# Performance work log

Hardware: AMD Instinct MI355X
Metric: run time of the kernel (lower is better)

Reference implementation:

```python
import jax, jax.numpy as jnp
import numpy as np

B, T, IN = 128, 2048, 32      # batch, seq_len, input dim
S, M = 32, 8                  # kaarma state dim, number of ensemble models
E, H = 64, 128                # encoder dim, controller GRU hidden
CIN = E + 1                   # controller input = [encoded, error]


def setup_inputs() -> dict:
    key = jax.random.key(0)
    ks = jax.random.split(key, 15)
    sc = 0.1  # small init scale keeps tanh/sigmoid in sane range
    return {
        "x": jax.random.normal(ks[0], (B, T, IN), jnp.float32),
        "y": jax.random.normal(ks[1], (B, T), jnp.float32),
        # mkaarma params: shared encoder + per-model recurrent state update
        "W_enc": jax.random.normal(ks[2], (IN, E), jnp.float32) * sc,
        "b_enc": jnp.zeros((E,), jnp.float32),
        "W_in": jax.random.normal(ks[3], (M, IN, S), jnp.float32) * sc,
        "W_rec": jax.random.normal(ks[4], (M, S, S), jnp.float32) * sc,
        "b_s": jnp.zeros((M, S), jnp.float32),
        # controller params: GRU cell + gate head
        "W_x": jax.random.normal(ks[5], (CIN, 3 * H), jnp.float32) * sc,
        "W_h": jax.random.normal(ks[6], (H, 3 * H), jnp.float32) * sc,
        "b_x": jnp.zeros((3 * H,), jnp.float32),
        "b_h": jnp.zeros((3 * H,), jnp.float32),
        "W_gate": jax.random.normal(ks[7], (H, M), jnp.float32) * sc,
        "b_gate": jnp.zeros((M,), jnp.float32),
    }


def reference(x, y, W_enc, b_enc, W_in, W_rec, b_s,
              W_x, W_h, b_x, b_h, W_gate, b_gate):
    Bv = x.shape[0]
    dt = x.dtype

    def step(carry, xy):
        kstate, h, err = carry            # [B,S], [B,H], [B]
        x_t, y_t = xy                     # [B,IN], [B]
        # mkaarma: encode input + ensemble of candidate next states
        encoded = jnp.tanh(x_t @ W_enc + b_enc)                        # [B,E]
        new_state = jnp.tanh(
            jnp.einsum('bi,mis->bms', x_t, W_in)
            + jnp.einsum('bs,msd->bmd', kstate, W_rec)
            + b_s
        )                                                              # [B,M,S]
        # controller: GRU cell on [encoded, error]
        inp = jnp.concatenate([encoded, err[:, None]], axis=1)         # [B,E+1]
        xz, xr, xn = jnp.split(inp @ W_x + b_x, 3, axis=1)
        hz, hr, hn = jnp.split(h @ W_h + b_h, 3, axis=1)
        z = jax.nn.sigmoid(xz + hz)
        r = jax.nn.sigmoid(xr + hr)
        n = jnp.tanh(xn + r * hn)
        h_new = (1.0 - z) * n + z * h                                  # [B,H]
        # gate softmax over models, mix candidate states
        gate = jax.nn.softmax(h_new @ W_gate + b_gate, axis=1)         # [B,M]
        kstate_new = jnp.einsum('bm,bms->bs', gate, new_state)         # [B,S]
        pred = kstate_new[:, -1]                                       # [B]
        err_new = pred - y_t
        return (kstate_new, h_new, err_new), pred

    init = (jnp.zeros((Bv, S), dt), jnp.zeros((Bv, H), dt), jnp.zeros((Bv,), dt))
    xs = (jnp.swapaxes(x, 0, 1), jnp.swapaxes(y, 0, 1))   # time-major
    _, preds = jax.lax.scan(step, init, xs)               # [T,B]
    return jnp.swapaxes(preds, 0, 1)                      # [B,T]
```

## Files before the change

### kernel.cpp

```cpp
#include <hip/hip_runtime.h>

typedef _Float16 h2 __attribute__((ext_vector_type(2)));
typedef _Float16 h8 __attribute__((ext_vector_type(8)));

#define NB 128
#define NT 2048
#define NIN 32
#define NS 32
#define NM 8
#define NE 64
#define NH 128
#define NH3 384

__device__ __forceinline__ h2 mkh2(float a, float b) {
  h2 r; r[0] = (_Float16)a; r[1] = (_Float16)b; return r;
}

template <int I>
__device__ __forceinline__ h2 pick2(h8 v) {
  return __builtin_shufflevector(v, v, 2 * I, 2 * I + 1);
}

__device__ __forceinline__ float fdot2(h2 a, h2 b, float c) {
#if __has_builtin(__builtin_amdgcn_fdot2)
  return __builtin_amdgcn_fdot2(a, b, c, false);
#else
  return c + (float)a[0] * (float)b[0] + (float)a[1] * (float)b[1];
#endif
}

__device__ __forceinline__ float rcpf(float v) {
#if __has_builtin(__builtin_amdgcn_rcpf)
  return __builtin_amdgcn_rcpf(v);
#else
  return 1.0f / v;
#endif
}

__device__ __forceinline__ float sigmoid_f(float v) { return rcpf(1.0f + __expf(-v)); }
__device__ __forceinline__ float tanh_f(float v) { return 1.0f - 2.0f * rcpf(1.0f + __expf(2.0f * v)); }

template <int CTRL>
__device__ __forceinline__ float dppadd(float v) {
  int t = __builtin_amdgcn_update_dpp(0, __float_as_int(v), CTRL, 0xF, 0xF, true);
  return v + __int_as_float(t);
}
__device__ __forceinline__ float wave_reduce63(float v) {
  v = dppadd<0x111>(v); v = dppadd<0x112>(v); v = dppadd<0x114>(v);
  v = dppadd<0x118>(v); v = dppadd<0x142>(v); v = dppadd<0x143>(v);
  return v;
}
__device__ __forceinline__ float pairsum(float v) {
  int t = __builtin_amdgcn_update_dpp(0, __float_as_int(v), 0xB1, 0xF, 0xF, true);
  return v + __int_as_float(t);
}

__device__ __forceinline__ void lds_fence() {
  asm volatile("s_waitcnt lgkmcnt(0)" ::: "memory");
}

__device__ __forceinline__ void softbar() {
  asm volatile("s_waitcnt lgkmcnt(0)\n\ts_barrier" ::: "memory");
}

#define RPW 16
__global__ __launch_bounds__(256, 1) void pre2(
    const float* __restrict__ gx, const float* __restrict__ W_enc,
    const float* __restrict__ b_enc, const float* __restrict__ W_x,
    const float* __restrict__ b_x, _Float16* __restrict__ xpre,
    _Float16* __restrict__ xh16, int t0, int CH) {
  const int tid = threadIdx.x, wv = tid >> 6, lane = tid & 63;
  __shared__ __align__(16) _Float16 x16[4][NIN];
  __shared__ __align__(16) _Float16 encA[4][RPW][NE];

  h2 we[16];
#pragma unroll
  for (int i = 0; i < 16; ++i)
    we[i] = mkh2(W_enc[(2 * i) * NE + lane], W_enc[(2 * i + 1) * NE + lane]);
  const float be = b_enc[lane];

  const int g0 = ((int)blockIdx.x * 4 + wv) * RPW;

  h2 wx3[96];
#pragma unroll 1
  for (int pass = 0; pass < 2; ++pass) {
#pragma unroll
    for (int kk = 0; kk < 3; ++kk) {
      const int j = lane + 64 * (3 * pass + kk);
#pragma unroll
      for (int i = 0; i < 32; ++i)
        wx3[kk * 32 + i] = mkh2(W_x[(size_t)(2 * i) * NH3 + j], W_x[(size_t)(2 * i + 1) * NH3 + j]);
    }
#pragma unroll 1
    for (int r = 0; r < RPW; ++r) {
      const int g = g0 + r;
      const int bb = g / CH, tc = g % CH;
      if (pass == 0) {
        const float* xr = gx + ((size_t)bb * NT + t0 + tc) * NIN;
        if (lane < NIN) x16[wv][lane] = (_Float16)xr[lane];
        lds_fence();
        if (lane < 16) {
          const unsigned v = *(const unsigned*)&x16[wv][2 * lane];
          ((unsigned*)xh16)[(size_t)g * 16 + lane] = v;
        }
        const h8* xv8 = (const h8*)x16[wv];
        float a = be;
#pragma unroll
        for (int i = 0; i < 4; ++i) {
          const h8 xv = xv8[i];
          a = fdot2(pick2<0>(xv), we[4 * i + 0], a);
          a = fdot2(pick2<1>(xv), we[4 * i + 1], a);
          a = fdot2(pick2<2>(xv), we[4 * i + 2], a);
          a = fdot2(pick2<3>(xv), we[4 * i + 3], a);
        }
        encA[wv][r][lane] = (_Float16)tanh_f(a);
        lds_fence();
      }
      const h8* ev8 = (const h8*)encA[wv][r];
      h8 ev[8];
#pragma unroll
      for (int i = 0; i < 8; ++i) ev[i] = ev8[i];
#pragma unroll
      for (int kk = 0; kk < 3; ++kk) {
        const int j = lane + 64 * (3 * pass + kk);
        float a = b_x[j], c = 0.f;
#pragma unroll
        for (int i = 0; i < 8; ++i) {
          a = fdot2(pick2<0>(ev[i]), wx3[kk * 32 + 4 * i + 0], a);
          c = fdot2(pick2<1>(ev[i]), wx3[kk * 32 + 4 * i + 1], c);
          a = fdot2(pick2<2>(ev[i]), wx3[kk * 32 + 4 * i + 2], a);
          c = fdot2(pick2<3>(ev[i]), wx3[kk * 32 + 4 * i + 3], c);
        }
        xpre[(size_t)g * NH3 + j] = (_Float16)(a + c);
      }
    }
  }
}

__global__ __launch_bounds__(384, 2) void rnn8(
    const float* __restrict__ gy, const _Float16* __restrict__ xpre,
    const _Float16* __restrict__ xh16,
    const float* __restrict__ W_h, const float* __restrict__ b_h,
    const float* __restrict__ W_in, const float* __restrict__ W_rec,
    const float* __restrict__ b_s, const float* __restrict__ W_x,
    const float* __restrict__ W_gate, const float* __restrict__ b_gate,
    float* __restrict__ out, float* __restrict__ state, int t0, int CH) {
  const int tid = threadIdx.x;
  const int b = blockIdx.x;
  const int wv = tid >> 6;
  const int lane = tid & 63;

  __shared__ __align__(16) _Float16 h_sh[2][NH];
  __shared__ __align__(16) _Float16 xpre_sh[2][NH3];
  __shared__ __align__(16) float ns_sh[2][NS][NM];
  __shared__ __align__(16) float xd_sh[2][2 * NH];
  __shared__ __align__(16) float gp_sh[2][4][NM];
  __shared__ __align__(16) _Float16 kst_sh[NS];
  __shared__ float err_sh;
  __shared__ float y_lds[NT];

  float* st = state + b * (NH + NS + 1);

  h2 wbig[96];
  h2 wrec[16];
  float wg[8];
  float bh[3], wxe[3];
  float bs4[4];
  float bg[8];
  float h_prev = 0.f;
  unsigned xpq[12];
  h8 xr0[4], xr1[4], xr2[4], xr3[4];

  const int gl = tid - 128;
  const int j = gl >> 1;
  const int half = gl & 1;

  for (int i = tid; i < CH; i += 384) y_lds[i] = gy[(size_t)b * NT + t0 + i];

  if (wv >= 2) {
#pragma unroll
    for (int g = 0; g < 3; ++g) {
      const int jc = j + 128 * g;
#pragma unroll
      for (int i = 0; i < 32; ++i)
        wbig[g * 32 + i] = mkh2(W_h[(size_t)(64 * half + 2 * i) * NH3 + jc],
                                W_h[(size_t)(64 * half + 2 * i + 1) * NH3 + jc]);
      bh[g] = b_h[jc];
      wxe[g] = W_x[(size_t)NE * NH3 + jc];
    }
#pragma unroll
    for (int m = 0; m < 8; ++m) wg[m] = half ? 0.f : W_gate[j * NM + m];
    {
      const int m0 = gl >> 5, d0 = gl & 31;
#pragma unroll
      for (int i = 0; i < 16; ++i)
        wrec[i] = mkh2(W_rec[m0 * 1024 + (2 * i) * 32 + d0],
                       W_rec[m0 * 1024 + (2 * i + 1) * 32 + d0]);
    }
    h_prev = t0 ? st[j] : 0.f;
    if (!half) h_sh[1][j] = (_Float16)h_prev;
  } else if (wv == 1) {
#pragma unroll
    for (int k = 0; k < 4; ++k) {
      const int o = lane + 64 * k, m = o >> 5, d = o & 31;
#pragma unroll
      for (int i = 0; i < 16; ++i)
        wbig[k * 16 + i] = mkh2(W_in[m * 1024 + (2 * i) * 32 + d],
                                W_in[m * 1024 + (2 * i + 1) * 32 + d]);
      bs4[k] = b_s[o];
    }
    {
      const h8* x0 = (const h8*)(xh16 + (size_t)(b * CH) * NIN);
#pragma unroll
      for (int i = 0; i < 4; ++i) xr0[i] = x0[i];
#pragma unroll
      for (int k = 0; k < 4; ++k) {
        float s = bs4[k];
#pragma unroll
        for (int i = 0; i < 4; ++i) {
          s = fdot2(pick2<0>(xr0[i]), wbig[k * 16 + 4 * i + 0], s);
          s = fdot2(pick2<1>(xr0[i]), wbig[k * 16 + 4 * i + 1], s);
          s = fdot2(pick2<2>(xr0[i]), wbig[k * 16 + 4 * i + 2], s);
          s = fdot2(pick2<3>(xr0[i]), wbig[k * 16 + 4 * i + 3], s);
        }
        xd_sh[1][lane + 64 * k] = s;
      }
    }
  } else {
#pragma unroll
    for (int m = 0; m < 8; ++m) bg[m] = b_gate[m];
    if (lane < NS) kst_sh[lane] = t0 ? (_Float16)st[NH + lane] : (_Float16)0.f;
    if (lane == 0) err_sh = t0 ? st[NH + NS] : 0.f;
  }
  __syncthreads();

  float hz = 0.f, hr = 0.f, hn = 0.f;

#define STEPK(K, XRK)                                                          \
  {                                                                            \
    const int tc = tc4 + (K);                                                  \
    const int q = (K) & 1, qp = q ^ 1;                                         \
                                 \
    if (wv >= 2) {                                                             \
      const h8* hv8 = (const h8*)&h_sh[qp][64 * half];                         \
      float a0 = 0.f, c0 = 0.f, a1 = 0.f, c1 = 0.f, a2 = 0.f, c2 = 0.f;        \
      _Pragma("unroll")                                                        \
      for (int i = 0; i < 8; ++i) {                                            \
        const h8 hv = hv8[i];                                                  \
        a0 = fdot2(pick2<0>(hv), wbig[4 * i + 0], a0);                         \
        c0 = fdot2(pick2<1>(hv), wbig[4 * i + 1], c0);                         \
        a0 = fdot2(pick2<2>(hv), wbig[4 * i + 2], a0);                         \
        c0 = fdot2(pick2<3>(hv), wbig[4 * i + 3], c0);                         \
        a1 = fdot2(pick2<0>(hv), wbig[32 + 4 * i + 0], a1);                    \
        c1 = fdot2(pick2<1>(hv), wbig[32 + 4 * i + 1], c1);                    \
        a1 = fdot2(pick2<2>(hv), wbig[32 + 4 * i + 2], a1);                    \
        c1 = fdot2(pick2<3>(hv), wbig[32 + 4 * i + 3], c1);                    \
        a2 = fdot2(pick2<0>(hv), wbig[64 + 4 * i + 0], a2);                    \
        c2 = fdot2(pick2<1>(hv), wbig[64 + 4 * i + 1], c2);                    \
        a2 = fdot2(pick2<2>(hv), wbig[64 + 4 * i + 2], a2);                    \
        c2 = fdot2(pick2<3>(hv), wbig[64 + 4 * i + 3], c2);                    \
      }                                                                        \
      hz = pairsum(a0 + c0) + bh[0];                                           \
      hr = pairsum(a1 + c1) + bh[1];                                           \
      hn = pairsum(a2 + c2) + bh[2];                                           \
    } else if (wv == 0) {                                                      \
      if (tc > 0) {                                                            \
        const int u = lane & 31;                                               \
        const float4* nsv = (const float4*)&ns_sh[qp][u][0];                   \
        const float4 n0 = nsv[0], n1 = nsv[1];                                 \
        const float4* g4 = (const float4*)&gp_sh[qp][0][0];                    \
        float4 A = g4[0], Bv = g4[1];                                          \
        A.x += g4[2].x + g4[4].x + g4[6].x; A.y += g4[2].y + g4[4].y + g4[6].y;\
        A.z += g4[2].z + g4[4].z + g4[6].z; A.w += g4[2].w + g4[4].w + g4[6].w;\
        Bv.x += g4[3].x + g4[5].x + g4[7].x; Bv.y += g4[3].y + g4[5].y + g4[7].y;\
        Bv.z += g4[3].z + g4[5].z + g4[7].z; Bv.w += g4[3].w + g4[5].w + g4[7].w;\
        float l[8] = {A.x + bg[0], A.y + bg[1], A.z + bg[2], A.w + bg[3],      \
                      Bv.x + bg[4], Bv.y + bg[5], Bv.z + bg[6], Bv.w + bg[7]}; \
        float mx = fmaxf(fmaxf(fmaxf(l[0], l[1]), fmaxf(l[2], l[3])),          \
                         fmaxf(fmaxf(l[4], l[5]), fmaxf(l[6], l[7])));         \
        float e[8], s = 0.f;                                                   \
        _Pragma("unroll")                                                      \
        for (int m = 0; m < 8; ++m) { e[m] = __expf(l[m] - mx); s += e[m]; }   \
        float ks = e[0] * n0.x + e[1] * n0.y + e[2] * n0.z + e[3] * n0.w +     \
                   e[4] * n1.x + e[5] * n1.y + e[6] * n1.z + e[7] * n1.w;      \
        ks *= rcpf(s);                                                         \
        if (lane < NS) kst_sh[u] = (_Float16)ks;                               \
        if (lane == 31) {                                                      \
          out[(size_t)b * NT + t0 + tc - 1] = ks;                              \
          err_sh = ks - y_lds[tc - 1];                                         \
        }                                                                      \
      }                                                                        \
    } else {    \
      if ((K) == 0) {                                                          \
        const unsigned* xpg = (const unsigned*)xpre;                           \
        _Pragma("unroll")                                                      \
        for (int k = 0; k < 4; ++k) {                                          \
          const size_t rr = (size_t)(b * CH + tc4 + k) * 192;                  \
          xpq[3 * k + 0] = xpg[rr + lane];                                     \
          xpq[3 * k + 1] = xpg[rr + lane + 64];                                \
          xpq[3 * k + 2] = xpg[rr + lane + 128];                               \
        }                                                                      \
        const h8* xg0 = (const h8*)(xh16 + (size_t)(b * CH + min(tc4 + 1, CH - 1)) * NIN); \
        const h8* xg1 = (const h8*)(xh16 + (size_t)(b * CH + min(tc4 + 2, CH - 1)) * NIN); \
        const h8* xg2 = (const h8*)(xh16 + (size_t)(b * CH + min(tc4 + 3, CH - 1)) * NIN); \
        const h8* xg3 = (const h8*)(xh16 + (size_t)(b * CH + min(tc4 + 4, CH - 1)) * NIN); \
        _Pragma("unroll")                                                      \
        for (int i = 0; i < 4; ++i) {                                          \
          xr0[i] = xg0[i]; xr1[i] = xg1[i]; xr2[i] = xg2[i]; xr3[i] = xg3[i];  \
        }                                                                      \
      }                                                                        \
      unsigned* xps = (unsigned*)&xpre_sh[q][0];                               \
      xps[lane] = xpq[3 * (K) + 0];                                            \
      xps[lane + 64] = xpq[3 * (K) + 1];                                       \
      xps[lane + 128] = xpq[3 * (K) + 2];                                      \
    }                                                                          \
    softbar();                                                                 \
                                 \
    if (wv >= 2) {                                                             \
      const float err = err_sh;                                                \
      const float xz = (float)xpre_sh[q][j] + err * wxe[0];                    \
      const float xr = (float)xpre_sh[q][j + 128] + err * wxe[1];              \
      const float xn = (float)xpre_sh[q][j + 256] + err * wxe[2];              \
      const float z = sigmoid_f(hz + xz);                                      \
      const float r = sigmoid_f(hr + xr);                                      \
      const float n = tanh_f(xn + r * hn);                                     \
      const float hnew = (1.f - z) * n + z * h_prev;                           \
      h_prev = hnew;                                                           \
      if (!half) h_sh[q][j] = (_Float16)hnew;                                  \
      float p[8];                                                              \
      _Pragma("unroll")                                                        \
      for (int m = 0; m < 8; ++m) p[m] = wave_reduce63(hnew * wg[m]);          \
      if (lane == 63) {                                                        \
        *(float4*)&gp_sh[q][wv - 2][0] = make_float4(p[0], p[1], p[2], p[3]);  \
        *(float4*)&gp_sh[q][wv - 2][4] = make_float4(p[4], p[5], p[6], p[7]);  \
      }                                                                        \
      const h8* kv8 = (const h8*)kst_sh;                                       \
      float s = xd_sh[qp][gl];                                                 \
      _Pragma("unroll")                                                        \
      for (int i = 0; i < 4; ++i) {                                            \
        const h8 kv = kv8[i];                                                  \
        s = fdot2(pick2<0>(kv), wrec[4 * i + 0], s);                           \
        s = fdot2(pick2<1>(kv), wrec[4 * i + 1], s);                           \
        s = fdot2(pick2<2>(kv), wrec[4 * i + 2], s);                           \
        s = fdot2(pick2<3>(kv), wrec[4 * i + 3], s);                           \
      }                                                                        \
      ns_sh[q][gl & 31][gl >> 5] = tanh_f(s);                                  \
    } else if (wv == 1) {                                                      \
      if (tc + 1 < CH) {                                                       \
        _Pragma("unroll")                                                      \
        for (int k = 0; k < 4; ++k) {                                          \
          float s = bs4[k];                                                    \
          _Pragma("unroll")                                                    \
          for (int i = 0; i < 4; ++i) {                                        \
            s = fdot2(pick2<0>(XRK[i]), wbig[k * 16 + 4 * i + 0], s);          \
            s = fdot2(pick2<1>(XRK[i]), wbig[k * 16 + 4 * i + 1], s);          \
            s = fdot2(pick2<2>(XRK[i]), wbig[k * 16 + 4 * i + 2], s);          \
            s = fdot2(pick2<3>(XRK[i]), wbig[k * 16 + 4 * i + 3], s);          \
          }                                                                    \
          xd_sh[q][lane + 64 * k] = s;                                         \
        }                                                                      \
      }                                                                        \
    }                                                                          \
    softbar();                                                                 \
  }

  for (int tc4 = 0; tc4 < CH; tc4 += 4) {
    STEPK(0, xr0)
    STEPK(1, xr1)
    STEPK(2, xr2)
    STEPK(3, xr3)
  }
#undef STEPK

  if (wv == 0) {
    const int qf = (CH - 1) & 1;
    const int u = lane & 31;
    const float4* nsv = (const float4*)&ns_sh[qf][u][0];
    const float4 n0 = nsv[0], n1 = nsv[1];
    const float4* g4 = (const float4*)&gp_sh[qf][0][0];
    float4 A = g4[0], Bv = g4[1];
    A.x += g4[2].x + g4[4].x + g4[6].x; A.y += g4[2].y + g4[4].y + g4[6].y;
    A.z += g4[2].z + g4[4].z + g4[6].z; A.w += g4[2].w + g4[4].w + g4[6].w;
    Bv.x += g4[3].x + g4[5].x + g4[7].x; Bv.y += g4[3].y + g4[5].y + g4[7].y;
    Bv.z += g4[3].z + g4[5].z + g4[7].z; Bv.w += g4[3].w + g4[5].w + g4[7].w;
    float l[8] = {A.x + bg[0], A.y + bg[1], A.z + bg[2], A.w + bg[3],
                  Bv.x + bg[4], Bv.y + bg[5], Bv.z + bg[6], Bv.w + bg[7]};
    float mx = fmaxf(fmaxf(fmaxf(l[0], l[1]), fmaxf(l[2], l[3])),
                     fmaxf(fmaxf(l[4], l[5]), fmaxf(l[6], l[7])));
    float e[8], s = 0.f;
#pragma unroll
    for (int m = 0; m < 8; ++m) { e[m] = __expf(l[m] - mx); s += e[m]; }
    float ks = e[0] * n0.x + e[1] * n0.y + e[2] * n0.z + e[3] * n0.w +
               e[4] * n1.x + e[5] * n1.y + e[6] * n1.z + e[7] * n1.w;
    ks *= rcpf(s);
    if (lane < NS) st[NH + u] = ks;
    if (lane == 31) {
      out[(size_t)b * NT + t0 + CH - 1] = ks;
      st[NH + NS] = ks - y_lds[CH - 1];
    }
  }
  if (wv >= 2 && !half) st[j] = h_prev;
}

extern "C" void kernel_launch(void* const* d_in, const int* in_sizes, int n_in,
                              void* d_out, int out_size, void* d_ws, size_t ws_size,
                              hipStream_t stream) {
  const float* x = (const float*)d_in[0];
  const float* y = (const float*)d_in[1];
  const float* W_enc = (const float*)d_in[2];
  const float* b_enc = (const float*)d_in[3];
  const float* W_in = (const float*)d_in[4];
  const float* W_rec = (const float*)d_in[5];
  const float* b_s = (const float*)d_in[6];
  const float* W_x = (const float*)d_in[7];
  const float* W_h = (const float*)d_in[8];
  const float* b_x = (const float*)d_in[9];
  const float* b_h = (const float*)d_in[10];
  const float* W_gate = (const float*)d_in[11];
  const float* b_gate = (const float*)d_in[12];
  float* out = (float*)d_out;

  const size_t stateB = (size_t)NB * (NH + NS + 1) * sizeof(float);
  int CH = NT;
  while (CH > 4) {
    const size_t need = (size_t)NB * CH * NH3 * 2 + (size_t)NB * CH * NIN * 2 + stateB;
    if (need <= ws_size) break;
    CH >>= 1;
  }

  _Float16* xpre = (_Float16*)d_ws;
  _Float16* xh16 = (_Float16*)((char*)d_ws + (size_t)NB * CH * NH3 * 2);
  float* state = (float*)((char*)d_ws + (size_t)NB * CH * NH3 * 2 + (size_t)NB * CH * NIN * 2);

  for (int t0 = 0; t0 < NT; t0 += CH) {
    pre2<<<dim3(2 * CH), dim3(256), 0, stream>>>(
        x, W_enc, b_enc, W_x, b_x, xpre, xh16, t0, CH);
    rnn8<<<dim3(NB), dim3(384), 0, stream>>>(
        y, xpre, xh16, W_h, b_h, W_in, W_rec, b_s, W_x, W_gate, b_gate,
        out, state, t0, CH);
  }
}
```

Measured before the change: 2.610 ms.

## Restructure recurrence to mix candidate states algebraically with one barrier per step

Replaces the warp-specialized 384-thread recurrent kernel with a uniform 256-thread kernel where each thread handles one GRU half-row and one (model, state) candidate. Instead of first forming the mixed state and then multiplying by W_rec, it applies W_rec to each model's previous candidate state and weights the results by the softmax gate (linearity), so the gate softmax, error, GRU and candidate update all fit into a single barrier per step. Inputs and precomputed projections are prefetched per thread four steps ahead into registers rather than staged through LDS by a loader wave. This trades 8x more recurrent dot-product work per thread and redundant per-thread softmax for removing a barrier and the serial dependency on the mixed state.

```diff
diff --git a/kernel.cpp b/kernel.cpp
--- a/kernel.cpp
+++ b/kernel.cpp
@@ -40,6 +40,12 @@
 __device__ __forceinline__ float sigmoid_f(float v) { return rcpf(1.0f + __expf(-v)); }
 __device__ __forceinline__ float tanh_f(float v) { return 1.0f - 2.0f * rcpf(1.0f + __expf(2.0f * v)); }
 
+__device__ __forceinline__ float f16bits_tof(unsigned short u) {
+  _Float16 h;
+  __builtin_memcpy(&h, &u, 2);
+  return (float)h;
+}
+
 template <int CTRL>
 __device__ __forceinline__ float dppadd(float v) {
   int t = __builtin_amdgcn_update_dpp(0, __float_as_int(v), CTRL, 0xF, 0xF, true);
@@ -58,7 +64,6 @@
 __device__ __forceinline__ void lds_fence() {
   asm volatile("s_waitcnt lgkmcnt(0)" ::: "memory");
 }
-
 __device__ __forceinline__ void softbar() {
   asm volatile("s_waitcnt lgkmcnt(0)\n\ts_barrier" ::: "memory");
 }
@@ -137,7 +142,7 @@
   }
 }
 
-__global__ __launch_bounds__(384, 2) void rnn8(
+__global__ __launch_bounds__(256, 1) void rnn9(
     const float* __restrict__ gy, const _Float16* __restrict__ xpre,
     const _Float16* __restrict__ xh16,
     const float* __restrict__ W_h, const float* __restrict__ b_h,
@@ -148,100 +153,114 @@
   const int tid = threadIdx.x;
   const int b = blockIdx.x;
   const int wv = tid >> 6;
-  const int lane = tid & 63;
+  const int j = tid >> 1;
+  const int half = tid & 1;
+  const int o = tid;
+  const int m0 = o >> 5, d0 = o & 31;
 
   __shared__ __align__(16) _Float16 h_sh[2][NH];
-  __shared__ __align__(16) _Float16 xpre_sh[2][NH3];
-  __shared__ __align__(16) float ns_sh[2][NS][NM];
-  __shared__ __align__(16) float xd_sh[2][2 * NH];
+  __shared__ __align__(16) _Float16 ns_sh[2][NM][NS];
+  __shared__ __align__(16) float ns31_sh[2][NM];
   __shared__ __align__(16) float gp_sh[2][4][NM];
-  __shared__ __align__(16) _Float16 kst_sh[NS];
-  __shared__ float err_sh;
   __shared__ float y_lds[NT];
-
-  float* st = state + b * (NH + NS + 1);
-
-  h2 wbig[96];
-  h2 wrec[16];
-  float wg[8];
-  float bh[3], wxe[3];
-  float bs4[4];
-  float bg[8];
-  float h_prev = 0.f;
-  unsigned xpq[12];
-  h8 xr0[4], xr1[4], xr2[4], xr3[4];
-
-  const int gl = tid - 128;
-  const int j = gl >> 1;
-  const int half = gl & 1;
-
-  for (int i = tid; i < CH; i += 384) y_lds[i] = gy[(size_t)b * NT + t0 + i];
-
-  if (wv >= 2) {
-#pragma unroll
-    for (int g = 0; g < 3; ++g) {
-      const int jc = j + 128 * g;
-#pragma unroll
-      for (int i = 0; i < 32; ++i)
-        wbig[g * 32 + i] = mkh2(W_h[(size_t)(64 * half + 2 * i) * NH3 + jc],
-                                W_h[(size_t)(64 * half + 2 * i + 1) * NH3 + jc]);
-      bh[g] = b_h[jc];
-      wxe[g] = W_x[(size_t)NE * NH3 + jc];
-    }
-#pragma unroll
-    for (int m = 0; m < 8; ++m) wg[m] = half ? 0.f : W_gate[j * NM + m];
-    {
-      const int m0 = gl >> 5, d0 = gl & 31;
-#pragma unroll
-      for (int i = 0; i < 16; ++i)
-        wrec[i] = mkh2(W_rec[m0 * 1024 + (2 * i) * 32 + d0],
-                       W_rec[m0 * 1024 + (2 * i + 1) * 32 + d0]);
-    }
-    h_prev = t0 ? st[j] : 0.f;
+  __shared__ float yprev_sh;
+
+  float* st = state + b * 420;
+
+  for (int i = tid; i < CH; i += 256) y_lds[i] = gy[(size_t)b * NT + t0 + i];
+
+  h2 wbig[96], wrec[16], win[16];
+  float wg[8], bg[8], bh3[3], wxe3[3];
+#pragma unroll
+  for (int g = 0; g < 3; ++g) {
+    const int jc = j + 128 * g;
+#pragma unroll
+    for (int i = 0; i < 32; ++i)
+      wbig[g * 32 + i] = mkh2(W_h[(size_t)(64 * half + 2 * i) * NH3 + jc],
+                              W_h[(size_t)(64 * half + 2 * i + 1) * NH3 + jc]);
+    bh3[g] = b_h[jc];
+    wxe3[g] = W_x[(size_t)NE * NH3 + jc];
+  }
+#pragma unroll
+  for (int m = 0; m < 8; ++m) {
+    wg[m] = half ? 0.f : W_gate[j * NM + m];
+    bg[m] = b_gate[m];
+  }
+#pragma unroll
+  for (int i = 0; i < 16; ++i) {
+    wrec[i] = mkh2(W_rec[m0 * 1024 + (2 * i) * 32 + d0],
+                   W_rec[m0 * 1024 + (2 * i + 1) * 32 + d0]);
+    win[i] = mkh2(W_in[m0 * 1024 + (2 * i) * 32 + d0],
+                  W_in[m0 * 1024 + (2 * i + 1) * 32 + d0]);
+  }
+  const float bs1 = b_s[o];
+
+  float h_prev, ns_last = 0.f;
+  if (t0 == 0) {
+    h_prev = 0.f;
+    if (!half) h_sh[1][j] = (_Float16)0.f;
+    ns_sh[1][m0][d0] = (_Float16)0.f;
+    if (d0 == 31) ns31_sh[1][m0] = 0.f;
+    if (tid < 32) ((float*)&gp_sh[1][0][0])[tid] = 0.f;
+    if (tid == 0) yprev_sh = 0.f;
+  } else {
+    h_prev = st[j];
     if (!half) h_sh[1][j] = (_Float16)h_prev;
-  } else if (wv == 1) {
-#pragma unroll
-    for (int k = 0; k < 4; ++k) {
-      const int o = lane + 64 * k, m = o >> 5, d = o & 31;
-#pragma unroll
-      for (int i = 0; i < 16; ++i)
-        wbig[k * 16 + i] = mkh2(W_in[m * 1024 + (2 * i) * 32 + d],
-                                W_in[m * 1024 + (2 * i + 1) * 32 + d]);
-      bs4[k] = b_s[o];
-    }
-    {
-      const h8* x0 = (const h8*)(xh16 + (size_t)(b * CH) * NIN);
-#pragma unroll
-      for (int i = 0; i < 4; ++i) xr0[i] = x0[i];
-#pragma unroll
-      for (int k = 0; k < 4; ++k) {
-        float s = bs4[k];
-#pragma unroll
-        for (int i = 0; i < 4; ++i) {
-          s = fdot2(pick2<0>(xr0[i]), wbig[k * 16 + 4 * i + 0], s);
-          s = fdot2(pick2<1>(xr0[i]), wbig[k * 16 + 4 * i + 1], s);
-          s = fdot2(pick2<2>(xr0[i]), wbig[k * 16 + 4 * i + 2], s);
-          s = fdot2(pick2<3>(xr0[i]), wbig[k * 16 + 4 * i + 3], s);
-        }
-        xd_sh[1][lane + 64 * k] = s;
-      }
-    }
-  } else {
-#pragma unroll
-    for (int m = 0; m < 8; ++m) bg[m] = b_gate[m];
-    if (lane < NS) kst_sh[lane] = t0 ? (_Float16)st[NH + lane] : (_Float16)0.f;
-    if (lane == 0) err_sh = t0 ? st[NH + NS] : 0.f;
+    const float nv = st[128 + o];
+    ns_sh[1][m0][d0] = (_Float16)nv;
+    if (d0 == 31) ns31_sh[1][m0] = nv;
+    if (tid < 32) ((float*)&gp_sh[1][0][0])[tid] = st[384 + tid];
+    if (tid == 0) yprev_sh = st[416];
+  }
+
+  h8 xrow[4][4];
+  unsigned short xp[4][3];
+#pragma unroll
+  for (int k = 0; k < 4; ++k) {
+    const int idx = min(k, CH - 1);
+    const h8* xr = (const h8*)(xh16 + (size_t)(b * CH + idx) * NIN);
+#pragma unroll
+    for (int i = 0; i < 4; ++i) xrow[k][i] = xr[i];
+    const unsigned short* xps =
+        (const unsigned short*)xpre + (size_t)(b * CH + idx) * NH3;
+    xp[k][0] = xps[j]; xp[k][1] = xps[j + 128]; xp[k][2] = xps[j + 256];
   }
   __syncthreads();
 
-  float hz = 0.f, hr = 0.f, hn = 0.f;
-
-#define STEPK(K, XRK)                                                          \
+#define STEP(K)                                                                \
   {                                                                            \
     const int tc = tc4 + (K);                                                  \
     const int q = (K) & 1, qp = q ^ 1;                                         \
-                                 \
-    if (wv >= 2) {                                                             \
+        \
+    float l[8];                                                                \
+    {                                                                          \
+      const float4* g4 = (const float4*)&gp_sh[qp][0][0];                      \
+      float4 A = g4[0], Bv = g4[1];                                            \
+      A.x += g4[2].x + g4[4].x + g4[6].x; A.y += g4[2].y + g4[4].y + g4[6].y;  \
+      A.z += g4[2].z + g4[4].z + g4[6].z; A.w += g4[2].w + g4[4].w + g4[6].w;  \
+      Bv.x += g4[3].x + g4[5].x + g4[7].x; Bv.y += g4[3].y + g4[5].y + g4[7].y;\
+      Bv.z += g4[3].z + g4[5].z + g4[7].z; Bv.w += g4[3].w + g4[5].w + g4[7].w;\
+      l[0] = A.x + bg[0]; l[1] = A.y + bg[1]; l[2] = A.z + bg[2];              \
+      l[3] = A.w + bg[3]; l[4] = Bv.x + bg[4]; l[5] = Bv.y + bg[5];            \
+      l[6] = Bv.z + bg[6]; l[7] = Bv.w + bg[7];                                \
+    }                                                                          \
+    float mx = fmaxf(fmaxf(fmaxf(l[0], l[1]), fmaxf(l[2], l[3])),              \
+                     fmaxf(fmaxf(l[4], l[5]), fmaxf(l[6], l[7])));             \
+    float e[8], s = 0.f;                                                       \
+    _Pragma("unroll")                                                          \
+    for (int m = 0; m < 8; ++m) { e[m] = __expf(l[m] - mx); s += e[m]; }       \
+    const float rs = rcpf(s);                                                  \
+                                                  \
+    float ks = 0.f;                                                            \
+    _Pragma("unroll")                                                          \
+    for (int m = 0; m < 8; ++m) ks += e[m] * ns31_sh[qp][m];                   \
+    ks *= rs;                                                                  \
+    const float yv = (tc == 0) ? yprev_sh : y_lds[tc - 1];                     \
+    const float err = ks - yv;                                                 \
+    if (tid == 0 && tc > 0) out[(size_t)b * NT + t0 + tc - 1] = ks;            \
+                                      \
+    float hz, hr, hn;                                                          \
+    {                                                                          \
       const h8* hv8 = (const h8*)&h_sh[qp][64 * half];                         \
       float a0 = 0.f, c0 = 0.f, a1 = 0.f, c1 = 0.f, a2 = 0.f, c2 = 0.f;        \
       _Pragma("unroll")                                                        \
@@ -260,69 +279,48 @@
         a2 = fdot2(pick2<2>(hv), wbig[64 + 4 * i + 2], a2);                    \
         c2 = fdot2(pick2<3>(hv), wbig[64 + 4 * i + 3], c2);                    \
       }                                                                        \
-      hz = pairsum(a0 + c0) + bh[0];                                           \
-      hr = pairsum(a1 + c1) + bh[1];                                           \
-      hn = pairsum(a2 + c2) + bh[2];                                           \
-    } else if (wv == 0) {                                                      \
-      if (tc > 0) {                                                            \
-        const int u = lane & 31;                                               \
-        const float4* nsv = (const float4*)&ns_sh[qp][u][0];                   \
-        const float4 n0 = nsv[0], n1 = nsv[1];                                 \
-        const float4* g4 = (const float4*)&gp_sh[qp][0][0];                    \
-        float4 A = g4[0], Bv = g4[1];                                          \
-        A.x += g4[2].x + g4[4].x + g4[6].x; A.y += g4[2].y + g4[4].y + g4[6].y;\
-        A.z += g4[2].z + g4[4].z + g4[6].z; A.w += g4[2].w + g4[4].w + g4[6].w;\
-        Bv.x += g4[3].x + g4[5].x + g4[7].x; Bv.y += g4[3].y + g4[5].y + g4[7].y;\
-        Bv.z += g4[3].z + g4[5].z + g4[7].z; Bv.w += g4[3].w + g4[5].w + g4[7].w;\
-        float l[8] = {A.x + bg[0], A.y + bg[1], A.z + bg[2], A.w + bg[3],      \
-                      Bv.x + bg[4], Bv.y + bg[5], Bv.z + bg[6], Bv.w + bg[7]}; \
-        float mx = fmaxf(fmaxf(fmaxf(l[0], l[1]), fmaxf(l[2], l[3])),          \
-                         fmaxf(fmaxf(l[4], l[5]), fmaxf(l[6], l[7])));         \
-        float e[8], s = 0.f;                                                   \
-        _Pragma("unroll")                                                      \
-        for (int m = 0; m < 8; ++m) { e[m] = __expf(l[m] - mx); s += e[m]; }   \
-        float ks = e[0] * n0.x + e[1] * n0.y + e[2] * n0.z + e[3] * n0.w +     \
-                   e[4] * n1.x + e[5] * n1.y + e[6] * n1.z + e[7] * n1.w;      \
-        ks *= rcpf(s);                                                         \
-        if (lane < NS) kst_sh[u] = (_Float16)ks;                               \
-        if (lane == 31) {                                                      \
-          out[(size_t)b * NT + t0 + tc - 1] = ks;                              \
-          err_sh = ks - y_lds[tc - 1];                                         \
-        }                                                                      \
+      hz = pairsum(a0 + c0) + bh3[0];                                          \
+      hr = pairsum(a1 + c1) + bh3[1];                                          \
+      hn = pairsum(a2 + c2) + bh3[2];                                          \
+    }                                                                          \
+                     \
+    float nsacc = 0.f;                                                         \
+    _Pragma("unroll")                                                          \
+    for (int mm = 0; mm < 8; ++mm) {                                           \
+      const h8* nr = (const h8*)&ns_sh[qp][mm][0];                             \
+      float qa = 0.f, qc = 0.f;                                                \
+      _Pragma("unroll")                                                        \
+      for (int i = 0; i < 4; ++i) {                                            \
+        const h8 nv = nr[i];                                                   \
+        qa = fdot2(pick2<0>(nv), wrec[4 * i + 0], qa);                         \
+        qc = fdot2(pick2<1>(nv), wrec[4 * i + 1], qc);                         \
+        qa = fdot2(pick2<2>(nv), wrec[4 * i + 2], qa);                         \
+        qc = fdot2(pick2<3>(nv), wrec[4 * i + 3], qc);                         \
       }                                                                        \
-    } else {    \
-      if ((K) == 0) {                                                          \
-        const unsigned* xpg = (const unsigned*)xpre;                           \
-        _Pragma("unroll")                                                      \
-        for (int k = 0; k < 4; ++k) {                                          \
-          const size_t rr = (size_t)(b * CH + tc4 + k) * 192;                  \
-          xpq[3 * k + 0] = xpg[rr + lane];                                     \
-          xpq[3 * k + 1] = xpg[rr + lane + 64];                                \
-          xpq[3 * k + 2] = xpg[rr + lane + 128];                               \
-        }                                                                      \
-        const h8* xg0 = (const h8*)(xh16 + (size_t)(b * CH + min(tc4 + 1, CH - 1)) * NIN); \
-        const h8* xg1 = (const h8*)(xh16 + (size_t)(b * CH + min(tc4 + 2, CH - 1)) * NIN); \
-        const h8* xg2 = (const h8*)(xh16 + (size_t)(b * CH + min(tc4 + 3, CH - 1)) * NIN); \
-        const h8* xg3 = (const h8*)(xh16 + (size_t)(b * CH + min(tc4 + 4, CH - 1)) * NIN); \
-        _Pragma("unroll")                                                      \
-        for (int i = 0; i < 4; ++i) {                                          \
-          xr0[i] = xg0[i]; xr1[i] = xg1[i]; xr2[i] = xg2[i]; xr3[i] = xg3[i];  \
-        }                                                                      \
-      }                                                                        \
-      unsigned* xps = (unsigned*)&xpre_sh[q][0];                               \
-      xps[lane] = xpq[3 * (K) + 0];                                            \
-      xps[lane + 64] = xpq[3 * (K) + 1];                                       \
-      xps[lane + 128] = xpq[3 * (K) + 2];                                      \
-    }                                                                          \
-    softbar();                                                                 \
-                                 \
-    if (wv >= 2) {                                                             \
-      const float err = err_sh;                                                \
-      const float xz = (float)xpre_sh[q][j] + err * wxe[0];                    \
-      const float xr = (float)xpre_sh[q][j + 128] + err * wxe[1];              \
-      const float xn = (float)xpre_sh[q][j + 256] + err * wxe[2];              \
+      nsacc += (e[mm] * rs) * (qa + qc);                                       \
+    }                                                                          \
+                                                            \
+    float xd = bs1;                                                            \
+    _Pragma("unroll")                                                          \
+    for (int i = 0; i < 4; ++i) {                                              \
+      const h8 xv = xrow[K][i];                                                \
+      xd = fdot2(pick2<0>(xv), win[4 * i + 0], xd);                            \
+      xd = fdot2(pick2<1>(xv), win[4 * i + 1], xd);                            \
+      xd = fdot2(pick2<2>(xv), win[4 * i + 2], xd);                            \
+      xd = fdot2(pick2<3>(xv), win[4 * i + 3], xd);                            \
+    }                                                                          \
+                                                                 \
+    const float nsv = tanh_f(xd + nsacc);                                      \
+    ns_sh[q][m0][d0] = (_Float16)nsv;                                          \
+    if (d0 == 31) ns31_sh[q][m0] = nsv;                                        \
+    ns_last = nsv;                                                             \
+                                                         \
+    {                                                                          \
+      const float xz = f16bits_tof(xp[K][0]) + err * wxe3[0];                  \
+      const float xr2 = f16bits_tof(xp[K][1]) + err * wxe3[1];                 \
+      const float xn = f16bits_tof(xp[K][2]) + err * wxe3[2];                  \
       const float z = sigmoid_f(hz + xz);                                      \
-      const float r = sigmoid_f(hr + xr);                                      \
+      const float r = sigmoid_f(hr + xr2);                                     \
       const float n = tanh_f(xn + r * hn);                                     \
       const float hnew = (1.f - z) * n + z * h_prev;                           \
       h_prev = hnew;                                                           \
@@ -330,76 +328,61 @@
       float p[8];                                                              \
       _Pragma("unroll")                                                        \
       for (int m = 0; m < 8; ++m) p[m] = wave_reduce63(hnew * wg[m]);          \
-      if (lane == 63) {                                                        \
-        *(float4*)&gp_sh[q][wv - 2][0] = make_float4(p[0], p[1], p[2], p[3]);  \
-        *(float4*)&gp_sh[q][wv - 2][4] = make_float4(p[4], p[5], p[6], p[7]);  \
+      if ((tid & 63) == 63) {                                                  \
+        *(float4*)&gp_sh[q][wv][0] = make_float4(p[0], p[1], p[2], p[3]);      \
+        *(float4*)&gp_sh[q][wv][4] = make_float4(p[4], p[5], p[6], p[7]);      \
       }                                                                        \
-      const h8* kv8 = (const h8*)kst_sh;                                       \
-      float s = xd_sh[qp][gl];                                                 \
+    }                                                                          \
+                                                   \
+    {                                                                          \
+      const int idx = min(tc + 4, CH - 1);                                     \
+      const h8* xr = (const h8*)(xh16 + (size_t)(b * CH + idx) * NIN);         \
       _Pragma("unroll")                                                        \
-      for (int i = 0; i < 4; ++i) {                                            \
-        const h8 kv = kv8[i];                                                  \
-        s = fdot2(pick2<0>(kv), wrec[4 * i + 0], s);                           \
-        s = fdot2(pick2<1>(kv), wrec[4 * i + 1], s);                           \
-        s = fdot2(pick2<2>(kv), wrec[4 * i + 2], s);                           \
-        s = fdot2(pick2<3>(kv), wrec[4 * i + 3], s);                           \
-      }                                                                        \
-      ns_sh[q][gl & 31][gl >> 5] = tanh_f(s);                                  \
-    } else if (wv == 1) {                                                      \
-      if (tc + 1 < CH) {                                                       \
-        _Pragma("unroll")                                                      \
-        for (int k = 0; k < 4; ++k) {                                          \
-          float s = bs4[k];                                                    \
-          _Pragma("unroll")                                                    \
-          for (int i = 0; i < 4; ++i) {                                        \
-            s = fdot2(pick2<0>(XRK[i]), wbig[k * 16 + 4 * i + 0], s);          \
-            s = fdot2(pick2<1>(XRK[i]), wbig[k * 16 + 4 * i + 1], s);          \
-            s = fdot2(pick2<2>(XRK[i]), wbig[k * 16 + 4 * i + 2], s);          \
-            s = fdot2(pick2<3>(XRK[i]), wbig[k * 16 + 4 * i + 3], s);          \
-          }                                                                    \
-          xd_sh[q][lane + 64 * k] = s;                                         \
-        }                                                                      \
-      }                                                                        \
+      for (int i = 0; i < 4; ++i) xrow[K][i] = xr[i];                          \
+      const unsigned short* xps =                                              \
+          (const unsigned short*)xpre + (size_t)(b * CH + idx) * NH3;          \
+      xp[K][0] = xps[j]; xp[K][1] = xps[j + 128]; xp[K][2] = xps[j + 256];     \
     }                                                                          \
     softbar();                                                                 \
   }
 
   for (int tc4 = 0; tc4 < CH; tc4 += 4) {
-    STEPK(0, xr0)
-    STEPK(1, xr1)
-    STEPK(2, xr2)
-    STEPK(3, xr3)
-  }
-#undef STEPK
-
-  if (wv == 0) {
-    const int qf = (CH - 1) & 1;
-    const int u = lane & 31;
-    const float4* nsv = (const float4*)&ns_sh[qf][u][0];
-    const float4 n0 = nsv[0], n1 = nsv[1];
+    STEP(0)
+    STEP(1)
+    STEP(2)
+    STEP(3)
+  }
+#undef STEP
+
+  const int qf = (CH - 1) & 1;
+  {
+    float l[8];
     const float4* g4 = (const float4*)&gp_sh[qf][0][0];
     float4 A = g4[0], Bv = g4[1];
     A.x += g4[2].x + g4[4].x + g4[6].x; A.y += g4[2].y + g4[4].y + g4[6].y;
     A.z += g4[2].z + g4[4].z + g4[6].z; A.w += g4[2].w + g4[4].w + g4[6].w;
     Bv.x += g4[3].x + g4[5].x + g4[7].x; Bv.y += g4[3].y + g4[5].y + g4[7].y;
     Bv.z += g4[3].z + g4[5].z + g4[7].z; Bv.w += g4[3].w + g4[5].w + g4[7].w;
-    float l[8] = {A.x + bg[0], A.y + bg[1], A.z + bg[2], A.w + bg[3],
-                  Bv.x + bg[4], Bv.y + bg[5], Bv.z + bg[6], Bv.w + bg[7]};
+    l[0] = A.x + bg[0]; l[1] = A.y + bg[1]; l[2] = A.z + bg[2];
+    l[3] = A.w + bg[3]; l[4] = Bv.x + bg[4]; l[5] = Bv.y + bg[5];
+    l[6] = Bv.z + bg[6]; l[7] = Bv.w + bg[7];
     float mx = fmaxf(fmaxf(fmaxf(l[0], l[1]), fmaxf(l[2], l[3])),
                      fmaxf(fmaxf(l[4], l[5]), fmaxf(l[6], l[7])));
     float e[8], s = 0.f;
 #pragma unroll
     for (int m = 0; m < 8; ++m) { e[m] = __expf(l[m] - mx); s += e[m]; }
-    float ks = e[0] * n0.x + e[1] * n0.y + e[2] * n0.z + e[3] * n0.w +
-               e[4] * n1.x + e[5] * n1.y + e[6] * n1.z + e[7] * n1.w;
+    float ks = 0.f;
+#pragma unroll
+    for (int m = 0; m < 8; ++m) ks += e[m] * ns31_sh[qf][m];
     ks *= rcpf(s);
-    if (lane < NS) st[NH + u] = ks;
-    if (lane == 31) {
+    if (tid == 0) {
       out[(size_t)b * NT + t0 + CH - 1] = ks;
-      st[NH + NS] = ks - y_lds[CH - 1];
+      st[416] = y_lds[CH - 1];
     }
   }
-  if (wv >= 2 && !half) st[j] = h_prev;
+  if (!half) st[j] = h_prev;
+  st[128 + o] = ns_last;
+  if (tid < 32) st[384 + tid] = ((const float*)&gp_sh[qf][0][0])[tid];
 }
 
 extern "C" void kernel_launch(void* const* d_in, const int* in_sizes, int n_in,
@@ -420,9 +403,9 @@
   const float* b_gate = (const float*)d_in[12];
   float* out = (float*)d_out;
 
-  const size_t stateB = (size_t)NB * (NH + NS + 1) * sizeof(float);
+  const size_t stateB = (size_t)NB * 420 * sizeof(float);
   int CH = NT;
-  while (CH > 4) {
+  while (CH > 8) {
     const size_t need = (size_t)NB * CH * NH3 * 2 + (size_t)NB * CH * NIN * 2 + stateB;
     if (need <= ws_size) break;
     CH >>= 1;
@@ -435,7 +418,7 @@
   for (int t0 = 0; t0 < NT; t0 += CH) {
     pre2<<<dim3(2 * CH), dim3(256), 0, stream>>>(
         x, W_enc, b_enc, W_x, b_x, xpre, xh16, t0, CH);
-    rnn8<<<dim3(NB), dim3(384), 0, stream>>>(
+    rnn9<<<dim3(NB), dim3(256), 0, stream>>>(
         y, xpre, xh16, W_h, b_h, W_in, W_rec, b_s, W_x, W_gate, b_gate,
         out, state, t0, CH);
   }
```

Measured after the change: 3.824 ms. +46.5%, slower.
